# Kernel optimization log

Measured on AMD Instinct MI355X. Metric: run time of the kernel, lower is better.

Reference implementation:

```python
import jax, jax.numpy as jnp
import numpy as np

SIG_G = [1.0, 1.0, 1.0]
LAYER_DIMS = [256, 128, 64]
N_ITER = 20
ALPHA = 0.01
B = 4096


def _cayley(g):
    # Cayley table C[a,b,c]: e_a * e_b = C[a,b,a^b] * e_{a^b} for diagonal metric g.
    n = len(g)
    nb = 1 << n
    C = np.zeros((nb, nb, nb), np.float32)
    for a in range(nb):
        for b in range(nb):
            # canonical reordering sign
            s = 0
            aa = a >> 1
            while aa:
                s += bin(aa & b).count('1')
                aa >>= 1
            sign = -1.0 if (s & 1) else 1.0
            # metric contribution from repeated generators
            for i in range(n):
                if (a >> i) & 1 and (b >> i) & 1:
                    sign *= g[i]
            C[a, b, a ^ b] = sign
    return jnp.asarray(C)


def _reverse_signs(n):
    # reverse: blade of grade k gets sign (-1)^(k*(k-1)/2)
    nb = 1 << n
    k = np.array([bin(i).count('1') for i in range(nb)])
    return jnp.asarray(((-1.0) ** (k * (k - 1) // 2)).astype(np.float32))


CAYLEY = _cayley(SIG_G)   # [8, 8, 8], sparse (one nonzero per (a,b))
REV = _reverse_signs(len(SIG_G))  # [8]


def _gp(x, W):
    # geometric product 'linear layer': x [B, Din, nb], W [Dout, Din, nb] -> [B, Dout, nb]
    return jnp.einsum('nja,ijb,abc->nic', x, W, CAYLEY, optimize=True)


def setup_inputs() -> dict:
    key = jax.random.key(0)
    ks = jax.random.split(key, 5)
    nb = 1 << len(SIG_G)
    x = jax.random.normal(ks[0], (B, LAYER_DIMS[0], nb), jnp.float32)
    W1 = jax.random.normal(ks[1], (LAYER_DIMS[0], LAYER_DIMS[1], nb), jnp.float32) * 0.01
    W2 = jax.random.normal(ks[2], (LAYER_DIMS[1], LAYER_DIMS[2], nb), jnp.float32) * 0.01
    h1 = jax.random.normal(ks[3], (B, LAYER_DIMS[1], nb), jnp.float32) * 0.001
    h2 = jax.random.normal(ks[4], (B, LAYER_DIMS[2], nb), jnp.float32) * 0.001
    return {'x': x, 'W1': W1, 'W2': W2, 'h1': h1, 'h2': h2}


def reference(x, W1, W2, h1, h2):
    states = [x, h1, h2]
    weights = [W1, W2]
    L = len(states)
    for _ in range(N_ITER):
        for l in range(1, L):
            W = weights[l - 1]                      # [D_{l-1}, D_l, nb]
            pred_prev = _gp(states[l], W)           # [B, D_{l-1}, nb]
            err_prev = states[l - 1] - pred_prev
            W_rev_T = jnp.transpose(W * REV, (1, 0, 2))  # reverse + transpose(0,1)
            grad = -_gp(err_prev, W_rev_T)          # [B, D_l, nb]
            if l < L - 1:
                pred_curr = _gp(states[l + 1], weights[l])
                grad = grad + (states[l] - pred_curr)
            grad = jnp.clip(grad, -1.0, 1.0)
            states[l] = states[l] - ALPHA * grad
    return tuple(states)
```

## Files before the change

kernel.cpp:

```cpp
#include <hip/hip_runtime.h>

#define N_ITER 20
#define ALPHA 0.01f

typedef unsigned short ushort_t;
typedef __attribute__((ext_vector_type(8))) short bf16x8;
typedef __attribute__((ext_vector_type(16))) float f32x16;

__device__ __forceinline__ float csign(int a, int b) {
    int s = 0;
    for (int aa = a >> 1; aa; aa >>= 1) s += __popc(aa & b);
    return (s & 1) ? -1.0f : 1.0f;
}

__device__ __forceinline__ float revsign(int b) {
    int k = __popc(b);
    return ((k * (k - 1) / 2) & 1) ? -1.0f : 1.0f;
}

__device__ __forceinline__ ushort_t f2bf(float f) {
    union { float f; unsigned u; } v;
    v.f = f;
    unsigned r = v.u + 0x7fffu + ((v.u >> 16) & 1u);
    return (ushort_t)(r >> 16);
}

__device__ __forceinline__ size_t swz64(int r, int k, int K) {
    return (size_t)r * K + (k & ~63) + ((((k >> 3) ^ r) & 7) << 3) + (k & 7);
}

__device__ __forceinline__ void async16(const void* g, void* l) {
    __builtin_amdgcn_global_load_lds((const __attribute__((address_space(1))) void*)g,
                                     (__attribute__((address_space(3))) void*)l, 16, 0, 0);
}

template <int N>
__device__ __forceinline__ void waitcnt_vm() {
    if constexpr (N == 0) asm volatile("s_waitcnt vmcnt(0)" ::: "memory");
    else if constexpr (N == 4) asm volatile("s_waitcnt vmcnt(4)" ::: "memory");
    else if constexpr (N == 6) asm volatile("s_waitcnt vmcnt(6)" ::: "memory");
    else if constexpr (N == 8) asm volatile("s_waitcnt vmcnt(8)" ::: "memory");
    else asm volatile("s_waitcnt vmcnt(0)" ::: "memory");
}

__global__ void build_M_kernel(const float* __restrict__ W, ushort_t* __restrict__ MfA,
                               ushort_t* __restrict__ Mrbt, ushort_t* __restrict__ Mrneg,
                               ushort_t* __restrict__ Mbtneg, int P, int Q) {
    int idx = blockIdx.x * blockDim.x + threadIdx.x;
    int total = P * Q * 64;
    if (idx >= total) return;
    int c = idx & 7;
    int a = (idx >> 3) & 7;
    int pq = idx >> 6;
    int q = pq % Q;
    int p = pq / Q;
    int b = a ^ c;
    float w = W[((size_t)p * Q + q) * 8 + b];
    float fw = csign(a, b) * w;
    float rw = csign(a, b) * revsign(b) * w;
    MfA[swz64(q * 8 + a, p * 8 + c, P * 8)] = f2bf(fw);
    Mrbt[swz64(q * 8 + c, p * 8 + a, P * 8)] = f2bf(rw);
    if (Mrneg) Mrneg[swz64(q * 8 + c, p * 8 + a, P * 8)] = f2bf(-rw);
    if (Mbtneg) Mbtneg[swz64(p * 8 + c, q * 8 + a, Q * 8)] = f2bf(-fw);
}

__global__ void f2bf_swz_kernel(const float* __restrict__ in, ushort_t* __restrict__ out,
                                int n, int kshift) {
    int i = blockIdx.x * blockDim.x + threadIdx.x;
    if (i >= n) return;
    int K = 1 << kshift;
    int r = i >> kshift;
    int k = i & (K - 1);
    out[swz64(r, k, K)] = f2bf(in[i]);
}

template <int MODE, int BM, int BN, bool ADDI>
__global__ __launch_bounds__(256) void gemm_k(const ushort_t* __restrict__ A,
                                              const ushort_t* __restrict__ BT, int K,
                                              const ushort_t* __restrict__ A2,
                                              const ushort_t* __restrict__ BT2, int K2,
                                              const float* __restrict__ Xf,
                                              const float* __restrict__ Rf,
                                              float* __restrict__ Hout,
                                              ushort_t* __restrict__ Bout,
                                              float* __restrict__ Fout, int N, int ypx) {
    constexpr int FI = BM / 64;
    constexpr int FJ = BN / 64;
    constexpr int CPW = (BM + BN) / 32;
    constexpr int SZ = (BM + BN) * 64;

    __shared__ ushort_t S[3 * SZ];

    const int wg = blockIdx.x;
    const int xcd = wg & 7;
    const int idx = wg >> 3;
    const int by = xcd * ypx + idx % ypx;
    const int bx = idx / ypx;

    const int t = threadIdx.x;
    const int lane = t & 63;
    const int w = t >> 6;
    const int wr = w >> 1;
    const int wc = w & 1;
    const int l31 = lane & 31;
    const int lh = lane >> 5;
    const int row0 = by * BM;
    const int col0 = bx * BN;
    const int srow = lane >> 3;
    const int sk = (lane & 7) * 8;
    const int sw7 = l31 & 7;

    f32x16 acc[FI][FJ];
#pragma unroll
    for (int i = 0; i < FI; ++i)
#pragma unroll
        for (int j = 0; j < FJ; ++j)
#pragma unroll
            for (int r = 0; r < 16; ++r) acc[i][j][r] = 0.0f;

    const ushort_t* gpA[CPW];
    const ushort_t* gpB[CPW];
    int lofs[CPW];
#pragma unroll
    for (int cc = 0; cc < CPW; ++cc) {
        int ch = cc * 4 + w;
        int r8 = ch * 8;
        lofs[cc] = ch * 512;
        if (r8 < BM) {
            gpA[cc] = A + (size_t)(row0 + r8 + srow) * K + sk;
            gpB[cc] = A2 ? (A2 + (size_t)(row0 + r8 + srow) * K2 + sk) : A;
        } else {
            gpA[cc] = BT + (size_t)(col0 + r8 - BM + srow) * K + sk;
            gpB[cc] = BT2 ? (BT2 + (size_t)(col0 + r8 - BM + srow) * K2 + sk) : BT;
        }
    }

    const int T1 = K >> 6;
    const int T2 = K2 >> 6;
    const int Ttot = T1 + T2;

    auto stage = [&](int tt, ushort_t* Sb) {
        if (tt < T1) {
#pragma unroll
            for (int cc = 0; cc < CPW; ++cc)
                async16(gpA[cc] + (size_t)tt * 64, &Sb[lofs[cc]]);
        } else {
            const int tl = tt - T1;
#pragma unroll
            for (int cc = 0; cc < CPW; ++cc)
                async16(gpB[cc] + (size_t)tl * 64, &Sb[lofs[cc]]);
        }
    };

    ushort_t* B0 = S;
    ushort_t* B1 = S + SZ;
    ushort_t* B2 = S + 2 * SZ;
    stage(0, B0);
    if (Ttot > 1) stage(1, B1);

    for (int tt = 0; tt < Ttot; ++tt) {
        if (tt + 1 < Ttot) {
            waitcnt_vm<CPW>();
        } else {
            waitcnt_vm<0>();
        }
        __builtin_amdgcn_s_barrier();
        __builtin_amdgcn_sched_barrier(0);

        if (tt + 2 < Ttot) stage(tt + 2, B2);

        bf16x8 af[4][FI], bfm[4][FJ];
#pragma unroll
        for (int s = 0; s < 4; ++s) {
            int pos = ((2 * s + lh) ^ sw7) * 8;
#pragma unroll
            for (int i = 0; i < FI; ++i)
                af[s][i] = *(const bf16x8*)&B0[(wr * (BM / 2) + i * 32 + l31) * 64 + pos];
#pragma unroll
            for (int j = 0; j < FJ; ++j)
                bfm[s][j] = *(const bf16x8*)&B0[(BM + wc * (BN / 2) + j * 32 + l31) * 64 + pos];
        }
#pragma unroll
        for (int s = 0; s < 4; ++s)
#pragma unroll
            for (int i = 0; i < FI; ++i)
#pragma unroll
                for (int j = 0; j < FJ; ++j)
                    acc[i][j] = __builtin_amdgcn_mfma_f32_32x32x16_bf16(af[s][i], bfm[s][j],
                                                                        acc[i][j], 0, 0, 0);
        ushort_t* tmp = B0; B0 = B1; B1 = B2; B2 = tmp;
    }

#pragma unroll
    for (int i = 0; i < FI; ++i) {
#pragma unroll
        for (int j = 0; j < FJ; ++j) {
#pragma unroll
            for (int r = 0; r < 16; ++r) {
                int row = row0 + wr * (BM / 2) + i * 32 + (r & 3) + 8 * (r >> 2) + 4 * lh;
                int col = col0 + wc * (BN / 2) + j * 32 + l31;
                size_t off = (size_t)row * N + col;
                float v = acc[i][j][r];
                if (MODE == 1) {
                    Fout[off] = v;
                } else if (MODE == 2) {
                    float h = Xf[off];
                    float g = fminf(fmaxf(v - Rf[off], -1.0f), 1.0f);
                    float hn = h - ALPHA * g;
                    Hout[off] = hn;
                    Bout[swz64(row, col, N)] = f2bf(hn);
                } else if (MODE == 3) {
                    float h = Xf[off];
                    float g = fminf(fmaxf(v, -1.0f), 1.0f);
                    float hn = h - ALPHA * g;
                    Hout[off] = hn;
                    Bout[swz64(row, col, N)] = f2bf(hn);
                } else {
                    float vv = v + ((ADDI && row == col) ? 1.0f : 0.0f);
                    Bout[swz64(col, row, N)] = f2bf(vv);
                }
            }
        }
    }
}

extern "C" void kernel_launch(void* const* d_in, const int* in_sizes, int n_in,
                              void* d_out, int out_size, void* d_ws, size_t ws_size,
                              hipStream_t stream) {
    const float* X  = (const float*)d_in[0];
    const float* W1 = (const float*)d_in[1];
    const float* W2 = (const float*)d_in[2];
    const float* h1 = (const float*)d_in[3];
    const float* h2 = (const float*)d_in[4];
    float* out = (float*)d_out;

    const size_t szX  = (size_t)4096 * 2048;
    const size_t szH1 = (size_t)4096 * 1024;
    const size_t szH2 = (size_t)4096 * 512;

    float* outX = out;
    float* H1 = out + szX;
    float* H2 = H1 + szH1;

    ushort_t* M1fwdA  = (ushort_t*)d_ws;
    ushort_t* M1rbt   = M1fwdA + (size_t)1024 * 2048;
    ushort_t* M2fwdA  = M1rbt + (size_t)1024 * 2048;
    ushort_t* M2rbt   = M2fwdA + (size_t)512 * 1024;
    ushort_t* M2rneg  = M2rbt + (size_t)512 * 1024;
    ushort_t* M2btneg = M2rneg + (size_t)512 * 1024;
    ushort_t* GmT1p   = M2btneg + (size_t)1024 * 512;
    ushort_t* GmT2    = GmT1p + (size_t)1024 * 1024;
    ushort_t* Xb      = GmT2 + (size_t)512 * 512;
    ushort_t* H1bA    = Xb + szX;
    ushort_t* H1bB    = H1bA + szH1;
    ushort_t* H2bA    = H1bB + szH1;
    ushort_t* H2bB    = H2bA + szH2;
    float*    R       = (float*)(H2bB + szH2);

    build_M_kernel<<<(256 * 128 * 64 + 255) / 256, 256, 0, stream>>>(
        W1, M1fwdA, M1rbt, nullptr, nullptr, 256, 128);
    build_M_kernel<<<(128 * 64 * 64 + 255) / 256, 256, 0, stream>>>(
        W2, M2fwdA, M2rbt, M2rneg, M2btneg, 128, 64);

    hipMemcpyAsync(H1, h1, szH1 * sizeof(float), hipMemcpyDeviceToDevice, stream);
    hipMemcpyAsync(H2, h2, szH2 * sizeof(float), hipMemcpyDeviceToDevice, stream);
    f2bf_swz_kernel<<<(int)((szX + 255) / 256), 256, 0, stream>>>(X, Xb, (int)szX, 11);
    f2bf_swz_kernel<<<(int)((szH1 + 255) / 256), 256, 0, stream>>>(h1, H1bA, (int)szH1, 10);
    f2bf_swz_kernel<<<(int)((szH2 + 255) / 256), 256, 0, stream>>>(h2, H2bA, (int)szH2, 9);

    gemm_k<1, 128, 64, false><<<dim3(16 * 32), 256, 0, stream>>>(
        Xb, M1rbt, 2048, nullptr, nullptr, 0, nullptr, nullptr, nullptr, nullptr, R, 1024, 4);
    gemm_k<4, 128, 64, true><<<dim3(16 * 8), 256, 0, stream>>>(
        M1fwdA, M1rbt, 2048, nullptr, nullptr, 0, nullptr, nullptr, nullptr, GmT1p, nullptr, 1024, 1);
    gemm_k<4, 64, 64, false><<<dim3(8 * 8), 256, 0, stream>>>(
        M2fwdA, M2rbt, 1024, nullptr, nullptr, 0, nullptr, nullptr, nullptr, GmT2, nullptr, 512, 1);

    ushort_t* H1old = H1bA; ushort_t* H1new = H1bB;
    ushort_t* H2old = H2bA; ushort_t* H2new = H2bB;
    for (int it = 0; it < N_ITER; ++it) {
        gemm_k<2, 128, 64, false><<<dim3(16 * 32), 256, 0, stream>>>(
            H1old, GmT1p, 1024, H2old, M2btneg, 512, H1, R, H1, H1new, nullptr, 1024, 4);
        gemm_k<3, 64, 64, false><<<dim3(8 * 64), 256, 0, stream>>>(
            H2old, GmT2, 512, H1new, M2rneg, 1024, H2, nullptr, H2, H2new, nullptr, 512, 8);
        ushort_t* tmp;
        tmp = H1old; H1old = H1new; H1new = tmp;
        tmp = H2old; H2old = H2new; H2new = tmp;
    }

    hipMemcpyAsync(outX, X, szX * sizeof(float), hipMemcpyDeviceToDevice, stream);
}
```

Before: 1.015 ms.

## Drop fp32 state traffic by reading state from staged bf16 A tile

The update kernels no longer read and write fp32 hidden states every iteration. The previous state value is taken from the bf16 copy already staged in LDS when the K-tile index equals the column-block index, the residual R is stored as bf16, and fp32 outputs are written only on the last iteration. Tile sizes for the H1 update and the precompute GEMMs also drop from 128x64 to 64x64 to raise the block count. This removes a large share of global memory traffic per iteration, but the states now accumulate in bf16 across iterations, which costs precision, and hcap adds register pressure.

```diff
diff --git a/kernel.cpp b/kernel.cpp
--- a/kernel.cpp
+++ b/kernel.cpp
@@ -23,6 +23,12 @@
     v.f = f;
     unsigned r = v.u + 0x7fffu + ((v.u >> 16) & 1u);
     return (ushort_t)(r >> 16);
+}
+
+__device__ __forceinline__ float bf2f(ushort_t h) {
+    union { unsigned u; float f; } v;
+    v.u = ((unsigned)h) << 16;
+    return v.f;
 }
 
 __device__ __forceinline__ size_t swz64(int r, int k, int K) {
@@ -79,11 +85,10 @@
                                               const ushort_t* __restrict__ BT, int K,
                                               const ushort_t* __restrict__ A2,
                                               const ushort_t* __restrict__ BT2, int K2,
-                                              const float* __restrict__ Xf,
-                                              const float* __restrict__ Rf,
-                                              float* __restrict__ Hout,
+                                              const ushort_t* __restrict__ Rb,
+                                              float* __restrict__ Ffinal,
                                               ushort_t* __restrict__ Bout,
-                                              float* __restrict__ Fout, int N, int ypx) {
+                                              int N, int ypx) {
     constexpr int FI = BM / 64;
     constexpr int FJ = BN / 64;
     constexpr int CPW = (BM + BN) / 32;
@@ -118,6 +123,12 @@
 #pragma unroll
             for (int r = 0; r < 16; ++r) acc[i][j][r] = 0.0f;
 
+    float hcap[FI][16];
+#pragma unroll
+    for (int i = 0; i < FI; ++i)
+#pragma unroll
+        for (int r = 0; r < 16; ++r) hcap[i][r] = 0.0f;
+
     const ushort_t* gpA[CPW];
     const ushort_t* gpB[CPW];
     int lofs[CPW];
@@ -167,6 +178,22 @@
         __builtin_amdgcn_s_barrier();
         __builtin_amdgcn_sched_barrier(0);
 
+        if constexpr (MODE == 2 || MODE == 3) {
+            if (tt == bx) {
+                const int kc = wc * (BN / 2) + l31;
+#pragma unroll
+                for (int i = 0; i < FI; ++i) {
+#pragma unroll
+                    for (int r = 0; r < 16; ++r) {
+                        int lrow = wr * (BM / 2) + i * 32 + (r & 3) + 8 * (r >> 2) + 4 * lh;
+                        ushort_t hv =
+                            B0[lrow * 64 + ((((kc >> 3) ^ lrow) & 7) << 3) + (kc & 7)];
+                        hcap[i][r] = bf2f(hv);
+                    }
+                }
+            }
+        }
+
         if (tt + 2 < Ttot) stage(tt + 2, B2);
 
         bf16x8 af[4][FI], bfm[4][FJ];
@@ -199,22 +226,20 @@
             for (int r = 0; r < 16; ++r) {
                 int row = row0 + wr * (BM / 2) + i * 32 + (r & 3) + 8 * (r >> 2) + 4 * lh;
                 int col = col0 + wc * (BN / 2) + j * 32 + l31;
-                size_t off = (size_t)row * N + col;
                 float v = acc[i][j][r];
                 if (MODE == 1) {
-                    Fout[off] = v;
+                    Bout[swz64(row, col, N)] = f2bf(v);
                 } else if (MODE == 2) {
-                    float h = Xf[off];
-                    float g = fminf(fmaxf(v - Rf[off], -1.0f), 1.0f);
-                    float hn = h - ALPHA * g;
-                    Hout[off] = hn;
+                    float rb = bf2f(Rb[swz64(row, col, N)]);
+                    float g = fminf(fmaxf(v - rb, -1.0f), 1.0f);
+                    float hn = hcap[i][r] - ALPHA * g;
                     Bout[swz64(row, col, N)] = f2bf(hn);
+                    if (Ffinal) Ffinal[(size_t)row * N + col] = hn;
                 } else if (MODE == 3) {
-                    float h = Xf[off];
                     float g = fminf(fmaxf(v, -1.0f), 1.0f);
-                    float hn = h - ALPHA * g;
-                    Hout[off] = hn;
+                    float hn = hcap[i][r] - ALPHA * g;
                     Bout[swz64(row, col, N)] = f2bf(hn);
+                    if (Ffinal) Ffinal[(size_t)row * N + col] = hn;
                 } else {
                     float vv = v + ((ADDI && row == col) ? 1.0f : 0.0f);
                     Bout[swz64(col, row, N)] = f2bf(vv);
@@ -255,33 +280,34 @@
     ushort_t* H1bB    = H1bA + szH1;
     ushort_t* H2bA    = H1bB + szH1;
     ushort_t* H2bB    = H2bA + szH2;
-    float*    R       = (float*)(H2bB + szH2);
+    ushort_t* Rb      = H2bB + szH2;
 
     build_M_kernel<<<(256 * 128 * 64 + 255) / 256, 256, 0, stream>>>(
         W1, M1fwdA, M1rbt, nullptr, nullptr, 256, 128);
     build_M_kernel<<<(128 * 64 * 64 + 255) / 256, 256, 0, stream>>>(
         W2, M2fwdA, M2rbt, M2rneg, M2btneg, 128, 64);
 
-    hipMemcpyAsync(H1, h1, szH1 * sizeof(float), hipMemcpyDeviceToDevice, stream);
-    hipMemcpyAsync(H2, h2, szH2 * sizeof(float), hipMemcpyDeviceToDevice, stream);
     f2bf_swz_kernel<<<(int)((szX + 255) / 256), 256, 0, stream>>>(X, Xb, (int)szX, 11);
     f2bf_swz_kernel<<<(int)((szH1 + 255) / 256), 256, 0, stream>>>(h1, H1bA, (int)szH1, 10);
     f2bf_swz_kernel<<<(int)((szH2 + 255) / 256), 256, 0, stream>>>(h2, H2bA, (int)szH2, 9);
 
-    gemm_k<1, 128, 64, false><<<dim3(16 * 32), 256, 0, stream>>>(
-        Xb, M1rbt, 2048, nullptr, nullptr, 0, nullptr, nullptr, nullptr, nullptr, R, 1024, 4);
-    gemm_k<4, 128, 64, true><<<dim3(16 * 8), 256, 0, stream>>>(
-        M1fwdA, M1rbt, 2048, nullptr, nullptr, 0, nullptr, nullptr, nullptr, GmT1p, nullptr, 1024, 1);
+    gemm_k<1, 64, 64, false><<<dim3(16 * 64), 256, 0, stream>>>(
+        Xb, M1rbt, 2048, nullptr, nullptr, 0, nullptr, nullptr, Rb, 1024, 8);
+    gemm_k<4, 64, 64, true><<<dim3(16 * 16), 256, 0, stream>>>(
+        M1fwdA, M1rbt, 2048, nullptr, nullptr, 0, nullptr, nullptr, GmT1p, 1024, 2);
     gemm_k<4, 64, 64, false><<<dim3(8 * 8), 256, 0, stream>>>(
-        M2fwdA, M2rbt, 1024, nullptr, nullptr, 0, nullptr, nullptr, nullptr, GmT2, nullptr, 512, 1);
+        M2fwdA, M2rbt, 1024, nullptr, nullptr, 0, nullptr, nullptr, GmT2, 512, 1);
 
     ushort_t* H1old = H1bA; ushort_t* H1new = H1bB;
     ushort_t* H2old = H2bA; ushort_t* H2new = H2bB;
     for (int it = 0; it < N_ITER; ++it) {
-        gemm_k<2, 128, 64, false><<<dim3(16 * 32), 256, 0, stream>>>(
-            H1old, GmT1p, 1024, H2old, M2btneg, 512, H1, R, H1, H1new, nullptr, 1024, 4);
+        const bool last = (it == N_ITER - 1);
+        gemm_k<2, 64, 64, false><<<dim3(16 * 64), 256, 0, stream>>>(
+            H1old, GmT1p, 1024, H2old, M2btneg, 512, Rb, last ? H1 : nullptr,
+            H1new, 1024, 8);
         gemm_k<3, 64, 64, false><<<dim3(8 * 64), 256, 0, stream>>>(
-            H2old, GmT2, 512, H1new, M2rneg, 1024, H2, nullptr, H2, H2new, nullptr, 512, 8);
+            H2old, GmT2, 512, H1new, M2rneg, 1024, nullptr, last ? H2 : nullptr,
+            H2new, 512, 8);
         ushort_t* tmp;
         tmp = H1old; H1old = H1new; H1new = tmp;
         tmp = H2old; H2old = H2new; H2new = tmp;
```

Result: slower. 1.145 ms (+12.8%).

## Fuse iteration loop into persistent kernel with grid barriers and register-resident state

Applied to the files above, without the earlier changes.

Replaces the 40 per-iteration GEMM launches with one persistent kernel of 512 blocks. It uses a hierarchical atomic grid barrier between the H1 and H2 phases. The fp32 states h1 and h2 and the residual R stay in registers across iterations, and the fp32 outputs are written only on the last iteration. This removes launch overhead and repeated fp32 global reads and writes. In exchange it relies on all 512 blocks being co-resident (launch_bounds 256,2), and the spin barrier adds synchronisation cost.

```diff
diff --git a/kernel.cpp b/kernel.cpp
--- a/kernel.cpp
+++ b/kernel.cpp
@@ -74,28 +74,18 @@
     out[swz64(r, k, K)] = f2bf(in[i]);
 }
 
-template <int MODE, int BM, int BN, bool ADDI>
-__global__ __launch_bounds__(256) void gemm_k(const ushort_t* __restrict__ A,
-                                              const ushort_t* __restrict__ BT, int K,
-                                              const ushort_t* __restrict__ A2,
-                                              const ushort_t* __restrict__ BT2, int K2,
-                                              const float* __restrict__ Xf,
-                                              const float* __restrict__ Rf,
-                                              float* __restrict__ Hout,
-                                              ushort_t* __restrict__ Bout,
-                                              float* __restrict__ Fout, int N, int ypx) {
+template <int BM, int BN>
+__device__ __forceinline__ void gemm_core(f32x16 (&acc)[BM / 64][BN / 64],
+                                          ushort_t* __restrict__ S,
+                                          const ushort_t* __restrict__ A,
+                                          const ushort_t* __restrict__ BT, int K,
+                                          const ushort_t* __restrict__ A2,
+                                          const ushort_t* __restrict__ BT2, int K2,
+                                          int row0, int col0) {
     constexpr int FI = BM / 64;
     constexpr int FJ = BN / 64;
     constexpr int CPW = (BM + BN) / 32;
     constexpr int SZ = (BM + BN) * 64;
-
-    __shared__ ushort_t S[3 * SZ];
-
-    const int wg = blockIdx.x;
-    const int xcd = wg & 7;
-    const int idx = wg >> 3;
-    const int by = xcd * ypx + idx % ypx;
-    const int bx = idx / ypx;
 
     const int t = threadIdx.x;
     const int lane = t & 63;
@@ -104,13 +94,10 @@
     const int wc = w & 1;
     const int l31 = lane & 31;
     const int lh = lane >> 5;
-    const int row0 = by * BM;
-    const int col0 = bx * BN;
     const int srow = lane >> 3;
     const int sk = (lane & 7) * 8;
     const int sw7 = l31 & 7;
 
-    f32x16 acc[FI][FJ];
 #pragma unroll
     for (int i = 0; i < FI; ++i)
 #pragma unroll
@@ -190,37 +177,148 @@
                                                                         acc[i][j], 0, 0, 0);
         ushort_t* tmp = B0; B0 = B1; B1 = B2; B2 = tmp;
     }
-
-#pragma unroll
-    for (int i = 0; i < FI; ++i) {
-#pragma unroll
-        for (int j = 0; j < FJ; ++j) {
+}
+
+template <int MODE, int BM, int BN, bool ADDI>
+__global__ __launch_bounds__(256) void gemm_k(const ushort_t* __restrict__ A,
+                                              const ushort_t* __restrict__ BT, int K,
+                                              ushort_t* __restrict__ Bout,
+                                              float* __restrict__ Fout, int N, int ypx) {
+    __shared__ ushort_t S[3 * (BM + BN) * 64];
+    const int wg = blockIdx.x;
+    const int xcd = wg & 7;
+    const int idx = wg >> 3;
+    const int by = xcd * ypx + idx % ypx;
+    const int bx = idx / ypx;
+
+    f32x16 acc[BM / 64][BN / 64];
+    gemm_core<BM, BN>(acc, S, A, BT, K, nullptr, nullptr, 0, by * BM, bx * BN);
+
+    const int lane = threadIdx.x & 63;
+    const int w = threadIdx.x >> 6;
+    const int wr = w >> 1;
+    const int wc = w & 1;
+    const int l31 = lane & 31;
+    const int lh = lane >> 5;
+    const int row0 = by * BM;
+    const int col0 = bx * BN;
+
+#pragma unroll
+    for (int i = 0; i < BM / 64; ++i) {
+#pragma unroll
+        for (int j = 0; j < BN / 64; ++j) {
 #pragma unroll
             for (int r = 0; r < 16; ++r) {
                 int row = row0 + wr * (BM / 2) + i * 32 + (r & 3) + 8 * (r >> 2) + 4 * lh;
                 int col = col0 + wc * (BN / 2) + j * 32 + l31;
-                size_t off = (size_t)row * N + col;
                 float v = acc[i][j][r];
                 if (MODE == 1) {
-                    Fout[off] = v;
-                } else if (MODE == 2) {
-                    float h = Xf[off];
-                    float g = fminf(fmaxf(v - Rf[off], -1.0f), 1.0f);
-                    float hn = h - ALPHA * g;
-                    Hout[off] = hn;
-                    Bout[swz64(row, col, N)] = f2bf(hn);
-                } else if (MODE == 3) {
-                    float h = Xf[off];
-                    float g = fminf(fmaxf(v, -1.0f), 1.0f);
-                    float hn = h - ALPHA * g;
-                    Hout[off] = hn;
-                    Bout[swz64(row, col, N)] = f2bf(hn);
+                    Fout[(size_t)row * N + col] = v;
                 } else {
                     float vv = v + ((ADDI && row == col) ? 1.0f : 0.0f);
                     Bout[swz64(col, row, N)] = f2bf(vv);
                 }
             }
         }
+    }
+}
+
+__device__ __forceinline__ void grid_bar(unsigned* bar, unsigned k, int b) {
+    __syncthreads();
+    if (threadIdx.x == 0) {
+        __threadfence();
+        unsigned old = atomicAdd(&bar[(b >> 6) * 32], 1u);
+        if (old == 64u * k - 1u) {
+            unsigned ot = atomicAdd(&bar[8 * 32], 1u);
+            if (ot == 8u * k - 1u) atomicAdd(&bar[9 * 32], 1u);
+        }
+        while (atomicAdd(&bar[9 * 32], 0u) < k) __builtin_amdgcn_s_sleep(1);
+        __threadfence();
+    }
+    __syncthreads();
+}
+
+__global__ __launch_bounds__(256, 2) void pc_iter_kernel(
+    const ushort_t* __restrict__ GmT1p, const ushort_t* __restrict__ M2btneg,
+    const ushort_t* __restrict__ GmT2, const ushort_t* __restrict__ M2rneg,
+    ushort_t* __restrict__ H1b0, ushort_t* __restrict__ H1b1,
+    ushort_t* __restrict__ H2b0, ushort_t* __restrict__ H2b1,
+    const float* __restrict__ Rp, const float* __restrict__ h1in,
+    const float* __restrict__ h2in, float* __restrict__ H1out,
+    float* __restrict__ H2out, unsigned* bar) {
+    __shared__ ushort_t S[3 * (128 + 64) * 64];
+
+    const int b = blockIdx.x;
+    const int lane = threadIdx.x & 63;
+    const int w = threadIdx.x >> 6;
+    const int wr = w >> 1;
+    const int wc = w & 1;
+    const int l31 = lane & 31;
+    const int lh = lane >> 5;
+
+    const int rowA = ((b & 7) * 4 + ((b >> 3) & 3)) * 128;
+    const int colA = (b >> 5) * 64;
+    const int rowB = ((b & 7) * 8 + ((b >> 3) & 7)) * 64;
+    const int colB = (b >> 6) * 64;
+
+    float h1reg[2][16], rreg[2][16], h2reg[16];
+#pragma unroll
+    for (int i = 0; i < 2; ++i)
+#pragma unroll
+        for (int r = 0; r < 16; ++r) {
+            int row = rowA + wr * 64 + i * 32 + (r & 3) + 8 * (r >> 2) + 4 * lh;
+            int col = colA + wc * 32 + l31;
+            size_t off = (size_t)row * 1024 + col;
+            h1reg[i][r] = h1in[off];
+            rreg[i][r] = Rp[off];
+        }
+#pragma unroll
+    for (int r = 0; r < 16; ++r) {
+        int row = rowB + wr * 32 + (r & 3) + 8 * (r >> 2) + 4 * lh;
+        int col = colB + wc * 32 + l31;
+        h2reg[r] = h2in[(size_t)row * 512 + col];
+    }
+
+    ushort_t* h1rd = H1b0; ushort_t* h1wr = H1b1;
+    ushort_t* h2rd = H2b0; ushort_t* h2wr = H2b1;
+
+    unsigned k = 0;
+    for (int it = 0; it < N_ITER; ++it) {
+        {
+            f32x16 acc[2][1];
+            gemm_core<128, 64>(acc, S, h1rd, GmT1p, 1024, h2rd, M2btneg, 512, rowA, colA);
+#pragma unroll
+            for (int i = 0; i < 2; ++i)
+#pragma unroll
+                for (int r = 0; r < 16; ++r) {
+                    int row = rowA + wr * 64 + i * 32 + (r & 3) + 8 * (r >> 2) + 4 * lh;
+                    int col = colA + wc * 32 + l31;
+                    float g = fminf(fmaxf(acc[i][0][r] - rreg[i][r], -1.0f), 1.0f);
+                    h1reg[i][r] -= ALPHA * g;
+                    h1wr[swz64(row, col, 1024)] = f2bf(h1reg[i][r]);
+                    if (it == N_ITER - 1) H1out[(size_t)row * 1024 + col] = h1reg[i][r];
+                }
+        }
+        grid_bar(bar, ++k, b);
+
+        {
+            f32x16 acc[1][1];
+            gemm_core<64, 64>(acc, S, h2rd, GmT2, 512, h1wr, M2rneg, 1024, rowB, colB);
+#pragma unroll
+            for (int r = 0; r < 16; ++r) {
+                int row = rowB + wr * 32 + (r & 3) + 8 * (r >> 2) + 4 * lh;
+                int col = colB + wc * 32 + l31;
+                float g = fminf(fmaxf(acc[0][0][r], -1.0f), 1.0f);
+                h2reg[r] -= ALPHA * g;
+                h2wr[swz64(row, col, 512)] = f2bf(h2reg[r]);
+                if (it == N_ITER - 1) H2out[(size_t)row * 512 + col] = h2reg[r];
+            }
+        }
+        grid_bar(bar, ++k, b);
+
+        ushort_t* tmp;
+        tmp = h1rd; h1rd = h1wr; h1wr = tmp;
+        tmp = h2rd; h2rd = h2wr; h2wr = tmp;
     }
 }
 
@@ -256,36 +354,28 @@
     ushort_t* H2bA    = H1bB + szH1;
     ushort_t* H2bB    = H2bA + szH2;
     float*    R       = (float*)(H2bB + szH2);
+    unsigned* bar     = (unsigned*)(R + szH1);
+
+    hipMemsetAsync(bar, 0, 40 * 32 * sizeof(unsigned), stream);
 
     build_M_kernel<<<(256 * 128 * 64 + 255) / 256, 256, 0, stream>>>(
         W1, M1fwdA, M1rbt, nullptr, nullptr, 256, 128);
     build_M_kernel<<<(128 * 64 * 64 + 255) / 256, 256, 0, stream>>>(
         W2, M2fwdA, M2rbt, M2rneg, M2btneg, 128, 64);
 
-    hipMemcpyAsync(H1, h1, szH1 * sizeof(float), hipMemcpyDeviceToDevice, stream);
-    hipMemcpyAsync(H2, h2, szH2 * sizeof(float), hipMemcpyDeviceToDevice, stream);
     f2bf_swz_kernel<<<(int)((szX + 255) / 256), 256, 0, stream>>>(X, Xb, (int)szX, 11);
     f2bf_swz_kernel<<<(int)((szH1 + 255) / 256), 256, 0, stream>>>(h1, H1bA, (int)szH1, 10);
     f2bf_swz_kernel<<<(int)((szH2 + 255) / 256), 256, 0, stream>>>(h2, H2bA, (int)szH2, 9);
 
     gemm_k<1, 128, 64, false><<<dim3(16 * 32), 256, 0, stream>>>(
-        Xb, M1rbt, 2048, nullptr, nullptr, 0, nullptr, nullptr, nullptr, nullptr, R, 1024, 4);
+        Xb, M1rbt, 2048, nullptr, R, 1024, 4);
     gemm_k<4, 128, 64, true><<<dim3(16 * 8), 256, 0, stream>>>(
-        M1fwdA, M1rbt, 2048, nullptr, nullptr, 0, nullptr, nullptr, nullptr, GmT1p, nullptr, 1024, 1);
+        M1fwdA, M1rbt, 2048, GmT1p, nullptr, 1024, 1);
     gemm_k<4, 64, 64, false><<<dim3(8 * 8), 256, 0, stream>>>(
-        M2fwdA, M2rbt, 1024, nullptr, nullptr, 0, nullptr, nullptr, nullptr, GmT2, nullptr, 512, 1);
-
-    ushort_t* H1old = H1bA; ushort_t* H1new = H1bB;
-    ushort_t* H2old = H2bA; ushort_t* H2new = H2bB;
-    for (int it = 0; it < N_ITER; ++it) {
-        gemm_k<2, 128, 64, false><<<dim3(16 * 32), 256, 0, stream>>>(
-            H1old, GmT1p, 1024, H2old, M2btneg, 512, H1, R, H1, H1new, nullptr, 1024, 4);
-        gemm_k<3, 64, 64, false><<<dim3(8 * 64), 256, 0, stream>>>(
-            H2old, GmT2, 512, H1new, M2rneg, 1024, H2, nullptr, H2, H2new, nullptr, 512, 8);
-        ushort_t* tmp;
-        tmp = H1old; H1old = H1new; H1new = tmp;
-        tmp = H2old; H2old = H2new; H2new = tmp;
-    }
+        M2fwdA, M2rbt, 1024, GmT2, nullptr, 512, 1);
+
+    pc_iter_kernel<<<dim3(512), dim3(256), 0, stream>>>(
+        GmT1p, M2btneg, GmT2, M2rneg, H1bA, H1bB, H2bA, H2bB, R, h1, h2, H1, H2, bar);
 
     hipMemcpyAsync(outX, X, szX * sizeof(float), hipMemcpyDeviceToDevice, stream);
 }
```

Result: slower. 2.287 ms (+125.3%).
